# Optimization experiments

Hardware: AMD Instinct MI355X
Metric: run time of the kernel (lower is better)

The kernel has to match this reference:

```python
import jax, jax.numpy as jnp
import numpy as np
import math

B, N, D, H = 4, 2048, 1024, 16
DH = D // H  # dim per head
OUT = 1024

def setup_inputs() -> dict:
    key0 = jax.random.key(0)
    ks = jax.random.split(key0, 12)
    s = 1.0 / math.sqrt(D)
    return {
        "key": jax.random.normal(ks[0], (B, N, D), jnp.float32),
        "value": jax.random.normal(ks[1], (B, N, D), jnp.float32),
        "query": jax.random.normal(ks[2], (B, N, D), jnp.float32),
        "Wk": jax.random.normal(ks[3], (D, D), jnp.float32) * s,
        "bk": jax.random.normal(ks[4], (D,), jnp.float32) * 0.01,
        "Wv": jax.random.normal(ks[5], (D, D), jnp.float32) * s,
        "bv": jax.random.normal(ks[6], (D,), jnp.float32) * 0.01,
        "Wq": jax.random.normal(ks[7], (D, D), jnp.float32) * s,
        "bq": jax.random.normal(ks[8], (D,), jnp.float32) * 0.01,
        "Wo": jax.random.normal(ks[9], (D, OUT), jnp.float32) * s,
        "bo": jax.random.normal(ks[10], (OUT,), jnp.float32) * 0.01,
    }

def reference(key, value, query, Wk, bk, Wv, bv, Wq, bq, Wo, bo):
    scale = math.sqrt(DH)
    k = (key @ Wk + bk).reshape(B, N, H, DH).transpose(0, 2, 1, 3)    # [B,H,N,DH]
    v = (value @ Wv + bv).reshape(B, N, H, DH).transpose(0, 2, 1, 3)
    q = ((query @ Wq + bq) / scale).reshape(B, N, H, DH).transpose(0, 2, 1, 3)
    scores = jnp.einsum('bhqd,bhkd->bhqk', q, k).astype(jnp.float32)  # [B,H,N,N]
    attn = jax.nn.softmax(scores, axis=-1).astype(q.dtype)
    # dropout p=0.0 (eval / identity)
    ctx = jnp.einsum('bhqk,bhkd->bhqd', attn, v)                      # [B,H,N,DH]
    ctx = ctx.transpose(0, 2, 1, 3).reshape(B, N, D)
    out = ctx @ Wo + bo                                               # [B,N,OUT]
    return out
```

## Files before the change

### kernel.cpp

```cpp
#include <hip/hip_runtime.h>
#include <hip/hip_bf16.h>
#include <stdint.h>

#define BB 4
#define NN 2048
#define DD 1024
#define HH 16
#define DHH 64
#define MM (BB*NN)

typedef unsigned short u16;
typedef unsigned int u32;
typedef __bf16 bf16x8_t __attribute__((ext_vector_type(8)));
typedef float f32x4_t __attribute__((ext_vector_type(4)));
typedef float f32x16_t __attribute__((ext_vector_type(16)));

__device__ inline u16 f2b(float f) {
    __hip_bfloat16 h = __float2bfloat16(f);
    return *(u16*)&h;
}

__device__ inline u32 pack2(float lo, float hi) {
    __hip_bfloat162 h2 = __float22bfloat162_rn(make_float2(lo, hi));
    return *(u32*)&h2;
}

__device__ inline void gload16(const void* g, void* l) {
    __builtin_amdgcn_global_load_lds(
        (const __attribute__((address_space(1))) void*)g,
        (__attribute__((address_space(3))) void*)l, 16, 0, 0);
}

__global__ void cvt_kernel(const float* __restrict__ in, u16* __restrict__ out) {
    int i = (blockIdx.x * 256 + threadIdx.x) * 4;
    float4 v = *(const float4*)(in + i);
    ushort4 o;
    o.x = f2b(v.x); o.y = f2b(v.y); o.z = f2b(v.z); o.w = f2b(v.w);
    *(ushort4*)(out + i) = o;
}

__global__ void wtrans_kernel(const float* __restrict__ W0, const float* __restrict__ W1,
                              const float* __restrict__ W2, const float* __restrict__ W3,
                              u16* __restrict__ out_base) {
    int z = blockIdx.z;
    const float* W = (z == 0) ? W0 : (z == 1) ? W1 : (z == 2) ? W2 : W3;
    u16* o = out_base + (size_t)z * DD * DD;
    __shared__ float tile[64][65];
    int t = threadIdx.x;
    int r0 = t >> 6;
    int c = t & 63;
    int kb = blockIdx.x, nb = blockIdx.y;
#pragma unroll
    for (int i = 0; i < 16; ++i) {
        int r = i * 4 + r0;
        tile[r][c] = W[(size_t)(kb * 64 + r) * DD + nb * 64 + c];
    }
    __syncthreads();
#pragma unroll
    for (int i = 0; i < 16; ++i) {
        int r = i * 4 + r0;
        o[(size_t)(nb * 64 + r) * DD + kb * 64 + c] = f2b(tile[c][r]);
    }
}

template<int OUT_F32, int BIAS_ROW>
__global__ __launch_bounds__(256, 2)
void gemm_bt(const u16* __restrict__ A, const u16* __restrict__ Bt,
             const float* __restrict__ bias, void* __restrict__ Cout, float scale,
             size_t a_z, size_t bt_z, size_t c_z, int ldc) {
    __shared__ u16 As[2][128 * 64];
    __shared__ u16 Bs[2][128 * 64];
    const int t = threadIdx.x;
    const int w = t >> 6, l = t & 63;
    const int wm = w >> 1, wn = w & 1;
    const int g = l >> 4, c = l & 15;
    const int bm = blockIdx.x, bn = blockIdx.y, z = blockIdx.z;
    A += (size_t)z * a_z;
    Bt += (size_t)z * bt_z;

    const f32x4_t vzero = {0.f, 0.f, 0.f, 0.f};
    f32x4_t acc[4][4];
#pragma unroll
    for (int m = 0; m < 4; ++m)
#pragma unroll
        for (int n = 0; n < 4; ++n) acc[m][n] = vzero;

    const int srow = l >> 3;
    const int scol = ((l & 7) ^ srow) << 3;
    const int sa = (l & 7) << 4;

    const u16* ap[4];
    const u16* bp[4];
#pragma unroll
    for (int i = 0; i < 4; ++i) {
        const int chunk = w * 4 + i, row = chunk * 8 + srow;
        ap[i] = A + (size_t)(bm * 128 + row) * DD + scol;
        bp[i] = Bt + (size_t)(bn * 128 + row) * DD + scol;
    }

#define GSTAGE(buf_)                                                         \
    do {                                                                     \
        _Pragma("unroll")                                                    \
        for (int i_ = 0; i_ < 4; ++i_) {                                     \
            gload16(ap[i_], &As[buf_][(w * 4 + i_) * 512]);                  \
            gload16(bp[i_], &Bs[buf_][(w * 4 + i_) * 512]);                  \
            ap[i_] += 64; bp[i_] += 64;                                      \
        }                                                                    \
    } while (0)

    GSTAGE(0);

#pragma unroll 1
    for (int ks = 0; ks < 16; ++ks) {
        const int cur = ks & 1;
        if (ks < 15) {
            GSTAGE(cur ^ 1);
            asm volatile("s_waitcnt vmcnt(8)" ::: "memory");
        } else {
            asm volatile("s_waitcnt vmcnt(0)" ::: "memory");
        }
        __builtin_amdgcn_s_barrier();
        asm volatile("" ::: "memory");

        bf16x8_t af[4][2], bfr[4][2];
#pragma unroll
        for (int m = 0; m < 4; ++m) {
            int rowa = wm * 64 + m * 16 + c;
#pragma unroll
            for (int kk = 0; kk < 2; ++kk)
                af[m][kk] = *(const bf16x8_t*)&As[cur][rowa * 64 + (((kk * 64 + g * 16) ^ sa) >> 1)];
        }
#pragma unroll
        for (int n = 0; n < 4; ++n) {
            int rowb = wn * 64 + n * 16 + c;
#pragma unroll
            for (int kk = 0; kk < 2; ++kk)
                bfr[n][kk] = *(const bf16x8_t*)&Bs[cur][rowb * 64 + (((kk * 64 + g * 16) ^ sa) >> 1)];
        }
        __builtin_amdgcn_s_setprio(1);
#pragma unroll
        for (int kk = 0; kk < 2; ++kk)
#pragma unroll
            for (int m = 0; m < 4; ++m)
#pragma unroll
                for (int n = 0; n < 4; ++n)
                    acc[m][n] = __builtin_amdgcn_mfma_f32_16x16x32_bf16(
                        af[m][kk], bfr[n][kk], acc[m][n], 0, 0, 0);
        __builtin_amdgcn_s_setprio(0);

        asm volatile("" ::: "memory");
        __builtin_amdgcn_s_barrier();
        asm volatile("" ::: "memory");
    }
#undef GSTAGE

    char* Cz = (char*)Cout + (size_t)z * c_z * (OUT_F32 ? 4 : 2);
#pragma unroll
    for (int n = 0; n < 4; ++n) {
        int col = bn * 128 + wn * 64 + n * 16 + c;
        float bcol = BIAS_ROW ? 0.f : bias[col];
#pragma unroll
        for (int m = 0; m < 4; ++m) {
            int row = bm * 128 + wm * 64 + m * 16 + g * 4;
            float4 brow;
            if (BIAS_ROW) brow = *(const float4*)&bias[row];
#pragma unroll
            for (int j = 0; j < 4; ++j) {
                float bv = BIAS_ROW ? ((const float*)&brow)[j] : bcol;
                float v = (acc[m][n][j] + bv) * scale;
                if (OUT_F32)
                    ((float*)Cz)[(size_t)(row + j) * ldc + col] = v;
                else
                    ((u16*)Cz)[(size_t)(row + j) * ldc + col] = f2b(v);
            }
        }
    }
}

__global__ __launch_bounds__(256, 2)
void attn32_kernel(const u16* __restrict__ qb, const u16* __restrict__ kb,
                   const u16* __restrict__ vt, u16* __restrict__ ctx) {
    __shared__ u16 Kt[4][64 * 64];
    __shared__ u16 Vs[4][64 * 64];
    const int t = threadIdx.x;
    const int w = t >> 6, l = t & 63;
    const int hl = l >> 5, l31 = l & 31, l7 = l & 7, l3 = l >> 3;

    const int f = blockIdx.y * 8 + blockIdx.x;
    const int wg = (f & 7) * 64 + (f >> 3);
    const int qt = wg & 7, bh = wg >> 3;
    const int b = bh >> 4, h = bh & 15;
    const int hoff = h * DHH;
    const size_t kv0 = (size_t)b * NN;
    const size_t vt0 = (size_t)bh * DHH;

    const size_t qrow_base = (size_t)(b * NN + qt * 256 + w * 64);
    bf16x8_t qf[2][4];
#pragma unroll
    for (int qm = 0; qm < 2; ++qm)
#pragma unroll
        for (int dks = 0; dks < 4; ++dks)
            qf[qm][dks] = *(const bf16x8_t*)&qb[(qrow_base + qm * 32 + l31) * DD +
                                                hoff + dks * 16 + hl * 8];

    f32x16_t z16;
#pragma unroll
    for (int r = 0; r < 16; ++r) z16[r] = 0.f;

    f32x16_t accO[2][2];
#pragma unroll
    for (int qm = 0; qm < 2; ++qm)
#pragma unroll
        for (int dt = 0; dt < 2; ++dt) accO[qm][dt] = z16;
    f32x16_t lacc16[2];
    lacc16[0] = z16; lacc16[1] = z16;

    const int scol2 = (l7 ^ l3) << 3;
    const u16* kp[2];
    const u16* vp[2];
#pragma unroll
    for (int i = 0; i < 2; ++i) {
        const int ch = w * 2 + i, r = ch * 8 + l3, rr = (r >> 2) & 3;
        const int pr = (rr == 1 || rr == 2) ? (r ^ 12) : r;
        kp[i] = kb + (kv0 + pr) * DD + hoff + scol2;
        vp[i] = vt + (vt0 + r) * NN + scol2;
    }

#define STAGE(S_)                                                            \
    do {                                                                     \
        _Pragma("unroll")                                                    \
        for (int i_ = 0; i_ < 2; ++i_) {                                     \
            gload16(kp[i_], &Kt[S_][(w * 2 + i_) * 512]);                    \
            gload16(vp[i_], &Vs[S_][(w * 2 + i_) * 512]);                    \
        }                                                                    \
        _Pragma("unroll")                                                    \
        for (int i_ = 0; i_ < 2; ++i_) { kp[i_] += 64 * DD; vp[i_] += 64; }  \
    } while (0)

    STAGE(0);
    STAGE(1);
    STAGE(2);

#pragma unroll 1
    for (int kt = 0; kt < NN / 64; ++kt) {
        const int cur = kt & 3;
        if (kt < NN / 64 - 3) {
            STAGE((kt + 3) & 3);
            asm volatile("s_waitcnt vmcnt(12)" ::: "memory");
        } else if (kt == NN / 64 - 3) {
            asm volatile("s_waitcnt vmcnt(8)" ::: "memory");
        } else if (kt == NN / 64 - 2) {
            asm volatile("s_waitcnt vmcnt(4)" ::: "memory");
        } else {
            asm volatile("s_waitcnt vmcnt(0)" ::: "memory");
        }
        __builtin_amdgcn_s_barrier();
        asm volatile("" ::: "memory");

        const char* Kc = (const char*)Kt[cur];
        const char* Vc = (const char*)Vs[cur];

        bf16x8_t kf[2][4];
#pragma unroll
        for (int kt32 = 0; kt32 < 2; ++kt32)
#pragma unroll
            for (int dks = 0; dks < 4; ++dks)
                kf[kt32][dks] = *(const bf16x8_t*)(Kc + (kt32 * 32 + l31) * 128 +
                                                   ((dks * 32 + hl * 16) ^ (l7 << 4)));

        f32x16_t accS[2][2];
        __builtin_amdgcn_s_setprio(1);
#pragma unroll
        for (int qm = 0; qm < 2; ++qm)
#pragma unroll
            for (int kt32 = 0; kt32 < 2; ++kt32) {
                accS[qm][kt32] = __builtin_amdgcn_mfma_f32_32x32x16_bf16(
                    kf[kt32][0], qf[qm][0], z16, 0, 0, 0);
#pragma unroll
                for (int dks = 1; dks < 4; ++dks)
                    accS[qm][kt32] = __builtin_amdgcn_mfma_f32_32x32x16_bf16(
                        kf[kt32][dks], qf[qm][dks], accS[qm][kt32], 0, 0, 0);
            }
        __builtin_amdgcn_s_setprio(0);

#pragma unroll
        for (int qm = 0; qm < 2; ++qm) {
#pragma unroll
            for (int kt32 = 0; kt32 < 2; ++kt32)
#pragma unroll
                for (int r = 0; r < 16; ++r)
                    accS[qm][kt32][r] = __builtin_amdgcn_exp2f(accS[qm][kt32][r]);
            lacc16[qm] += accS[qm][0] + accS[qm][1];
        }

        bf16x8_t vf[4][2];
#pragma unroll
        for (int pm = 0; pm < 4; ++pm)
#pragma unroll
            for (int dt = 0; dt < 2; ++dt)
                vf[pm][dt] = *(const bf16x8_t*)(Vc + (dt * 32 + l31) * 128 +
                                                ((pm * 32 + hl * 16) ^ (l7 << 4)));

        __builtin_amdgcn_s_setprio(1);
#pragma unroll
        for (int qm = 0; qm < 2; ++qm)
#pragma unroll
            for (int pm = 0; pm < 4; ++pm) {
                const int kt32 = pm >> 1, half = pm & 1;
                union { u32 u[4]; bf16x8_t v; } pu;
#pragma unroll
                for (int j2 = 0; j2 < 4; ++j2)
                    pu.u[j2] = pack2(accS[qm][kt32][half * 8 + 2 * j2],
                                     accS[qm][kt32][half * 8 + 2 * j2 + 1]);
#pragma unroll
                for (int dt = 0; dt < 2; ++dt)
                    accO[qm][dt] = __builtin_amdgcn_mfma_f32_32x32x16_bf16(
                        vf[pm][dt], pu.v, accO[qm][dt], 0, 0, 0);
            }
        __builtin_amdgcn_s_setprio(0);

        asm volatile("" ::: "memory");
        __builtin_amdgcn_s_barrier();
        asm volatile("" ::: "memory");
    }
#undef STAGE

#pragma unroll
    for (int qm = 0; qm < 2; ++qm) {
        float s8[8];
#pragma unroll
        for (int r = 0; r < 8; ++r) s8[r] = lacc16[qm][r] + lacc16[qm][r + 8];
#pragma unroll
        for (int sl = 4; sl >= 1; sl >>= 1)
#pragma unroll
            for (int r = 0; r < sl; ++r) s8[r] += s8[r + sl];
        float rsum = s8[0] + __shfl_xor(s8[0], 32);
        const float rl = 1.0f / rsum;
        const size_t qrow = qrow_base + qm * 32 + l31;
#pragma unroll
        for (int dt = 0; dt < 2; ++dt)
#pragma unroll
            for (int m = 0; m < 4; ++m) {
                ushort4 o;
                o.x = f2b(accO[qm][dt][4 * m + 0] * rl);
                o.y = f2b(accO[qm][dt][4 * m + 1] * rl);
                o.z = f2b(accO[qm][dt][4 * m + 2] * rl);
                o.w = f2b(accO[qm][dt][4 * m + 3] * rl);
                *(ushort4*)&ctx[qrow * DD + hoff + dt * 32 + m * 8 + hl * 4] = o;
            }
    }
}

extern "C" void kernel_launch(void* const* d_in, const int* in_sizes, int n_in,
                              void* d_out, int out_size, void* d_ws, size_t ws_size,
                              hipStream_t stream) {
    (void)in_sizes; (void)n_in; (void)out_size; (void)ws_size;
    const float* key   = (const float*)d_in[0];
    const float* value = (const float*)d_in[1];
    const float* query = (const float*)d_in[2];
    const float* Wk = (const float*)d_in[3];
    const float* bk = (const float*)d_in[4];
    const float* Wv = (const float*)d_in[5];
    const float* bv = (const float*)d_in[6];
    const float* Wq = (const float*)d_in[7];
    const float* bq = (const float*)d_in[8];
    const float* Wo = (const float*)d_in[9];
    const float* bo = (const float*)d_in[10];

    char* ws = (char*)d_ws;
    const size_t MB = 1024 * 1024;
    u16* qbuf = (u16*)(ws + 0 * MB);
    u16* kbuf = (u16*)(ws + 16 * MB);
    u16* xb   = (u16*)(ws + 32 * MB);
    u16* WtK  = (u16*)(ws + 48 * MB);
    u16* WtV  = (u16*)(ws + 50 * MB);
    u16* WtQ  = (u16*)(ws + 52 * MB);
    u16* WtO  = (u16*)(ws + 54 * MB);
    u16* VT   = (u16*)(ws + 56 * MB);

    const int nelem = MM * DD;
    const int cvt_blocks = nelem / (256 * 4);

    wtrans_kernel<<<dim3(16, 16, 4), 256, 0, stream>>>(Wk, Wv, Wq, Wo, WtK);

    cvt_kernel<<<cvt_blocks, 256, 0, stream>>>(value, xb);
    gemm_bt<0, 1><<<dim3(8, 16, 4), 256, 0, stream>>>(
        WtV, xb, bv, VT, 1.0f, 0, (size_t)2048 * DD, (size_t)1024 * 2048, 2048);
    cvt_kernel<<<cvt_blocks, 256, 0, stream>>>(key, xb);
    gemm_bt<0, 0><<<dim3(64, 8, 1), 256, 0, stream>>>(
        xb, WtK, bk, kbuf, 1.0f, 0, 0, 0, DD);
    cvt_kernel<<<cvt_blocks, 256, 0, stream>>>(query, xb);
    gemm_bt<0, 0><<<dim3(64, 8, 1), 256, 0, stream>>>(
        xb, WtQ, bq, qbuf, 0.125f * 1.4426950408889634f, 0, 0, 0, DD);

    u16* ctx = xb;
    attn32_kernel<<<dim3(8, 64), 256, 0, stream>>>(qbuf, kbuf, VT, ctx);

    gemm_bt<1, 0><<<dim3(64, 8, 1), 256, 0, stream>>>(
        ctx, WtO, bo, d_out, 1.0f, 0, 0, 0, DD);
}
```

Measured before the change: 206.1 us.

## Split attention KV sequence across two wave groups with LDS reduction

```diff
diff --git a/kernel.cpp b/kernel.cpp
--- a/kernel.cpp
+++ b/kernel.cpp
@@ -177,13 +177,15 @@
     }
 }
 
-__global__ __launch_bounds__(256, 2)
+__global__ __launch_bounds__(512, 4)
 void attn32_kernel(const u16* __restrict__ qb, const u16* __restrict__ kb,
                    const u16* __restrict__ vt, u16* __restrict__ ctx) {
-    __shared__ u16 Kt[4][64 * 64];
-    __shared__ u16 Vs[4][64 * 64];
+    __shared__ u16 Kt[2][2][64 * 64];
+    __shared__ u16 Vs[2][2][64 * 64];
+    __shared__ float rx[4][2][64];
     const int t = threadIdx.x;
     const int w = t >> 6, l = t & 63;
+    const int ws = w & 3, half = w >> 2;
     const int hl = l >> 5, l31 = l & 31, l7 = l & 7, l3 = l >> 3;
 
     const int f = blockIdx.y * 8 + blockIdx.x;
@@ -191,10 +193,10 @@
     const int qt = wg & 7, bh = wg >> 3;
     const int b = bh >> 4, h = bh & 15;
     const int hoff = h * DHH;
-    const size_t kv0 = (size_t)b * NN;
+    const size_t kv0 = (size_t)b * NN + half * (NN / 2);
     const size_t vt0 = (size_t)bh * DHH;
 
-    const size_t qrow_base = (size_t)(b * NN + qt * 256 + w * 64);
+    const size_t qrow_base = (size_t)(b * NN + qt * 256 + ws * 64);
     bf16x8_t qf[2][4];
 #pragma unroll
     for (int qm = 0; qm < 2; ++qm)
@@ -220,36 +222,30 @@
     const u16* vp[2];
 #pragma unroll
     for (int i = 0; i < 2; ++i) {
-        const int ch = w * 2 + i, r = ch * 8 + l3, rr = (r >> 2) & 3;
+        const int ch = ws * 2 + i, r = ch * 8 + l3, rr = (r >> 2) & 3;
         const int pr = (rr == 1 || rr == 2) ? (r ^ 12) : r;
         kp[i] = kb + (kv0 + pr) * DD + hoff + scol2;
-        vp[i] = vt + (vt0 + r) * NN + scol2;
+        vp[i] = vt + (vt0 + r) * NN + half * (NN / 2) + scol2;
     }
 
 #define STAGE(S_)                                                            \
     do {                                                                     \
         _Pragma("unroll")                                                    \
         for (int i_ = 0; i_ < 2; ++i_) {                                     \
-            gload16(kp[i_], &Kt[S_][(w * 2 + i_) * 512]);                    \
-            gload16(vp[i_], &Vs[S_][(w * 2 + i_) * 512]);                    \
+            gload16(kp[i_], &Kt[half][S_][(ws * 2 + i_) * 512]);             \
+            gload16(vp[i_], &Vs[half][S_][(ws * 2 + i_) * 512]);             \
         }                                                                    \
         _Pragma("unroll")                                                    \
         for (int i_ = 0; i_ < 2; ++i_) { kp[i_] += 64 * DD; vp[i_] += 64; }  \
     } while (0)
 
     STAGE(0);
-    STAGE(1);
-    STAGE(2);
 
 #pragma unroll 1
-    for (int kt = 0; kt < NN / 64; ++kt) {
-        const int cur = kt & 3;
-        if (kt < NN / 64 - 3) {
-            STAGE((kt + 3) & 3);
-            asm volatile("s_waitcnt vmcnt(12)" ::: "memory");
-        } else if (kt == NN / 64 - 3) {
-            asm volatile("s_waitcnt vmcnt(8)" ::: "memory");
-        } else if (kt == NN / 64 - 2) {
+    for (int kt = 0; kt < NN / 128; ++kt) {
+        const int cur = kt & 1;
+        if (kt < NN / 128 - 1) {
+            STAGE(cur ^ 1);
             asm volatile("s_waitcnt vmcnt(4)" ::: "memory");
         } else {
             asm volatile("s_waitcnt vmcnt(0)" ::: "memory");
@@ -257,8 +253,8 @@
         __builtin_amdgcn_s_barrier();
         asm volatile("" ::: "memory");
 
-        const char* Kc = (const char*)Kt[cur];
-        const char* Vc = (const char*)Vs[cur];
+        const char* Kc = (const char*)Kt[half][cur];
+        const char* Vc = (const char*)Vs[half][cur];
 
         bf16x8_t kf[2][4];
 #pragma unroll
@@ -306,12 +302,12 @@
         for (int qm = 0; qm < 2; ++qm)
 #pragma unroll
             for (int pm = 0; pm < 4; ++pm) {
-                const int kt32 = pm >> 1, half = pm & 1;
+                const int kt32 = pm >> 1, halfp = pm & 1;
                 union { u32 u[4]; bf16x8_t v; } pu;
 #pragma unroll
                 for (int j2 = 0; j2 < 4; ++j2)
-                    pu.u[j2] = pack2(accS[qm][kt32][half * 8 + 2 * j2],
-                                     accS[qm][kt32][half * 8 + 2 * j2 + 1]);
+                    pu.u[j2] = pack2(accS[qm][kt32][halfp * 8 + 2 * j2],
+                                     accS[qm][kt32][halfp * 8 + 2 * j2 + 1]);
 #pragma unroll
                 for (int dt = 0; dt < 2; ++dt)
                     accO[qm][dt] = __builtin_amdgcn_mfma_f32_32x32x16_bf16(
@@ -325,6 +321,7 @@
     }
 #undef STAGE
 
+    float rsum[2];
 #pragma unroll
     for (int qm = 0; qm < 2; ++qm) {
         float s8[8];
@@ -334,20 +331,57 @@
         for (int sl = 4; sl >= 1; sl >>= 1)
 #pragma unroll
             for (int r = 0; r < sl; ++r) s8[r] += s8[r + sl];
-        float rsum = s8[0] + __shfl_xor(s8[0], 32);
-        const float rl = 1.0f / rsum;
-        const size_t qrow = qrow_base + qm * 32 + l31;
-#pragma unroll
-        for (int dt = 0; dt < 2; ++dt)
-#pragma unroll
-            for (int m = 0; m < 4; ++m) {
-                ushort4 o;
-                o.x = f2b(accO[qm][dt][4 * m + 0] * rl);
-                o.y = f2b(accO[qm][dt][4 * m + 1] * rl);
-                o.z = f2b(accO[qm][dt][4 * m + 2] * rl);
-                o.w = f2b(accO[qm][dt][4 * m + 3] * rl);
-                *(ushort4*)&ctx[qrow * DD + hoff + dt * 32 + m * 8 + hl * 4] = o;
-            }
+        rsum[qm] = s8[0] + __shfl_xor(s8[0], 32);
+    }
+
+    char* xbase = (ws < 2) ? ((char*)Kt + ws * 16384) : ((char*)Vs + (ws - 2) * 16384);
+    if (half == 1) {
+#pragma unroll
+        for (int qm = 0; qm < 2; ++qm)
+#pragma unroll
+            for (int dt = 0; dt < 2; ++dt)
+#pragma unroll
+                for (int j = 0; j < 4; ++j) {
+                    const int wq = (qm * 2 + dt) * 4 + j;
+                    *(uint4*)(xbase + wq * 1024 + ((l + wq) & 63) * 16) =
+                        ((const uint4*)&accO[qm][dt])[j];
+                }
+        rx[ws][0][l] = rsum[0];
+        rx[ws][1][l] = rsum[1];
+    }
+    __syncthreads();
+    if (half == 0) {
+#pragma unroll
+        for (int qm = 0; qm < 2; ++qm)
+#pragma unroll
+            for (int dt = 0; dt < 2; ++dt)
+#pragma unroll
+                for (int j = 0; j < 4; ++j) {
+                    const int wq = (qm * 2 + dt) * 4 + j;
+                    uint4 q = *(const uint4*)(xbase + wq * 1024 + ((l + wq) & 63) * 16);
+                    const float* qa = (const float*)&q;
+#pragma unroll
+                    for (int e = 0; e < 4; ++e) accO[qm][dt][j * 4 + e] += qa[e];
+                }
+        rsum[0] += rx[ws][0][l];
+        rsum[1] += rx[ws][1][l];
+
+#pragma unroll
+        for (int qm = 0; qm < 2; ++qm) {
+            const float rl = 1.0f / rsum[qm];
+            const size_t qrow = qrow_base + qm * 32 + l31;
+#pragma unroll
+            for (int dt = 0; dt < 2; ++dt)
+#pragma unroll
+                for (int m = 0; m < 4; ++m) {
+                    ushort4 o;
+                    o.x = f2b(accO[qm][dt][4 * m + 0] * rl);
+                    o.y = f2b(accO[qm][dt][4 * m + 1] * rl);
+                    o.z = f2b(accO[qm][dt][4 * m + 2] * rl);
+                    o.w = f2b(accO[qm][dt][4 * m + 3] * rl);
+                    *(ushort4*)&ctx[qrow * DD + hoff + dt * 32 + m * 8 + hl * 4] = o;
+                }
+        }
     }
 }
 
@@ -394,7 +428,7 @@
         xb, WtQ, bq, qbuf, 0.125f * 1.4426950408889634f, 0, 0, 0, DD);
 
     u16* ctx = xb;
-    attn32_kernel<<<dim3(8, 64), 256, 0, stream>>>(qbuf, kbuf, VT, ctx);
+    attn32_kernel<<<dim3(8, 64), 512, 0, stream>>>(qbuf, kbuf, VT, ctx);
 
     gemm_bt<1, 0><<<dim3(64, 8, 1), 256, 0, stream>>>(
         ctx, WtO, bo, d_out, 1.0f, 0, 0, 0, DD);
```

After: 724.9 us. +251.6%, slower.
